# Kernel tuning notes

Hardware: AMD Instinct MI355X
Metric: run time of the kernel (lower is better)

The kernel has to match this reference:

```python
import jax, jax.numpy as jnp
import numpy as np

EMB = 768
HEADS = 12
HD = EMB // HEADS
FF = 4 * EMB
EPS = 1e-5


def gelu_tanh(x):
    c = jnp.sqrt(jnp.asarray(2.0 / jnp.pi, x.dtype))
    return 0.5 * x * (1.0 + jnp.tanh(c * (x + 0.044715 * x ** 3)))


def layernorm(x, scale, shift):
    mean = x.mean(-1, keepdims=True)
    var = ((x - mean) ** 2).mean(-1, keepdims=True)
    return scale * (x - mean) / jnp.sqrt(var + EPS) + shift


def setup_inputs() -> dict:
    key = jax.random.key(0)
    ks = jax.random.split(key, 12)
    s = 0.02
    return {
        "x": jax.random.normal(ks[0], (8, 1024, EMB), jnp.float32),
        "Wq": jax.random.normal(ks[1], (EMB, EMB), jnp.float32) * s,
        "Wk": jax.random.normal(ks[2], (EMB, EMB), jnp.float32) * s,
        "Wv": jax.random.normal(ks[3], (EMB, EMB), jnp.float32) * s,
        "Wo": jax.random.normal(ks[4], (EMB, EMB), jnp.float32) * s,
        "bo": jnp.zeros((EMB,), jnp.float32),
        "W1": jax.random.normal(ks[5], (EMB, FF), jnp.float32) * s,
        "b1": jnp.zeros((FF,), jnp.float32),
        "W2": jax.random.normal(ks[6], (FF, EMB), jnp.float32) * s,
        "b2": jnp.zeros((EMB,), jnp.float32),
        "ln1_scale": jnp.ones((EMB,), jnp.float32),
        "ln1_shift": jnp.zeros((EMB,), jnp.float32),
        "ln2_scale": jnp.ones((EMB,), jnp.float32),
        "ln2_shift": jnp.zeros((EMB,), jnp.float32),
    }


def reference(x, Wq, Wk, Wv, Wo, bo, W1, b1, W2, b2,
              ln1_scale, ln1_shift, ln2_scale, ln2_shift):
    B, T, _ = x.shape
    inp = x
    h = layernorm(x, ln1_scale, ln1_shift)
    # QKV projections (no bias, qkv_bias=False)
    q = (h @ Wq).reshape(B, T, HEADS, HD).transpose(0, 2, 1, 3)  # [B,H,T,hd]
    k = (h @ Wk).reshape(B, T, HEADS, HD).transpose(0, 2, 1, 3)
    v = (h @ Wv).reshape(B, T, HEADS, HD).transpose(0, 2, 1, 3)
    scores = jnp.einsum('bhqd,bhkd->bhqk', q, k)
    causal = jnp.triu(jnp.ones((T, T), bool), k=1)
    scores = jnp.where(causal, -jnp.inf, scores)
    attn = jax.nn.softmax(scores / jnp.sqrt(jnp.asarray(HD, x.dtype)), axis=-1)
    ctx = jnp.einsum('bhqk,bhkd->bhqd', attn, v)
    ctx = ctx.transpose(0, 2, 1, 3).reshape(B, T, EMB)
    attn_out = ctx @ Wo + bo
    x = inp + attn_out  # dropout is identity (rate 0 / eval)
    inp = x
    h = layernorm(x, ln2_scale, ln2_shift)
    ff = gelu_tanh(h @ W1 + b1) @ W2 + b2
    return inp + ff
```

## Files before the change

### kernel.cpp

```cpp
#include <hip/hip_runtime.h>
#include <stdint.h>
#include <stddef.h>

#define EMB 768
#define FFD 3072
#define NHEAD 12
#define HD 64
#define SEQ 1024
#define NTOK 8192
#define QKVW 2304

typedef unsigned short u16;
typedef __attribute__((ext_vector_type(8))) short short8;
typedef __attribute__((ext_vector_type(4))) float f32x4;

__device__ __forceinline__ u16 f2bf(float f) {
  union { float f; uint32_t u; } w; w.f = f;
  uint32_t x = w.u + 0x7fffu + ((w.u >> 16) & 1u);
  return (u16)(x >> 16);
}

__device__ __forceinline__ void g2l16(const void* g, void* l) {
  __builtin_amdgcn_global_load_lds(
      (const __attribute__((address_space(1))) void*)g,
      (__attribute__((address_space(3))) void*)l, 16, 0, 0);
}

__global__ __launch_bounds__(256)
void transpose_kernel(const float* __restrict__ in, u16* __restrict__ out, int K, int N) {
  __shared__ float tile[32][33];
  const int n0 = blockIdx.x * 32, k0 = blockIdx.y * 32;
  const int tx = threadIdx.x & 31;
  const int ty = threadIdx.x >> 5;
#pragma unroll
  for (int i = 0; i < 32; i += 8)
    tile[ty + i][tx] = in[(size_t)(k0 + ty + i) * N + n0 + tx];
  __syncthreads();
#pragma unroll
  for (int i = 0; i < 32; i += 8)
    out[(size_t)(n0 + ty + i) * K + k0 + tx] = f2bf(tile[tx][ty + i]);
}

__global__ __launch_bounds__(256)
void transpose_qkv_kernel(const float* __restrict__ Wq, const float* __restrict__ Wk,
                          const float* __restrict__ Wv, u16* __restrict__ out) {
  __shared__ float tile[32][33];
  const float* in = blockIdx.z == 0 ? Wq : (blockIdx.z == 1 ? Wk : Wv);
  u16* o = out + (size_t)blockIdx.z * EMB * EMB;
  const int n0 = blockIdx.x * 32, k0 = blockIdx.y * 32;
  const int tx = threadIdx.x & 31;
  const int ty = threadIdx.x >> 5;
#pragma unroll
  for (int i = 0; i < 32; i += 8)
    tile[ty + i][tx] = in[(size_t)(k0 + ty + i) * EMB + n0 + tx];
  __syncthreads();
#pragma unroll
  for (int i = 0; i < 32; i += 8)
    o[(size_t)(n0 + ty + i) * EMB + k0 + tx] = f2bf(tile[tx][ty + i]);
}

__global__ __launch_bounds__(256)
void ln_kernel(const float* __restrict__ x, const float* __restrict__ sc,
               const float* __restrict__ sh, u16* __restrict__ out) {
  const int row = blockIdx.x;
  const int tid = threadIdx.x;
  const float* xr = x + (size_t)row * EMB;
  float v0 = xr[tid], v1 = xr[tid + 256], v2 = xr[tid + 512];
  float s = v0 + v1 + v2;
  float ss = v0 * v0 + v1 * v1 + v2 * v2;
#pragma unroll
  for (int m = 1; m < 64; m <<= 1) { s += __shfl_xor(s, m, 64); ss += __shfl_xor(ss, m, 64); }
  __shared__ float red[8];
  const int wave = tid >> 6, lane = tid & 63;
  if (lane == 0) { red[wave] = s; red[wave + 4] = ss; }
  __syncthreads();
  s = red[0] + red[1] + red[2] + red[3];
  ss = red[4] + red[5] + red[6] + red[7];
  const float mean = s * (1.f / EMB);
  const float var = ss * (1.f / EMB) - mean * mean;
  const float inv = rsqrtf(var + 1e-5f);
  u16* orow = out + (size_t)row * EMB;
  orow[tid]       = f2bf((v0 - mean) * inv * sc[tid]       + sh[tid]);
  orow[tid + 256] = f2bf((v1 - mean) * inv * sc[tid + 256] + sh[tid + 256]);
  orow[tid + 512] = f2bf((v2 - mean) * inv * sc[tid + 512] + sh[tid + 512]);
}

template <int EPI, int MT>
__global__ __launch_bounds__(256)
void gemm_kernel(const u16* __restrict__ A, const u16* __restrict__ BT,
                 void* __restrict__ Cp, const float* __restrict__ bias,
                 const float* __restrict__ res, int M, int N, int K) {
  constexpr int MI = MT / 32;
  __shared__ u16 As[MT * 64];
  __shared__ u16 Bs[128 * 64];

  const int nwg = gridDim.x * gridDim.y;
  const int orig = blockIdx.y * gridDim.x + blockIdx.x;
  const int swz = (orig & 7) * (nwg >> 3) + (orig >> 3);
  const int m0 = (swz / gridDim.x) * MT;
  const int n0 = (swz % gridDim.x) * 128;

  const int tid = threadIdx.x;
  const int wave = tid >> 6, lane = tid & 63;
  const int wr = wave >> 1, wc = wave & 1;
  const int r = lane & 15, g = lane >> 4;
  const int lrow = lane >> 3;
  const int lelem = (lane & 7) * 8;

  f32x4 acc[MI][4] = {};

  const int nkt = K >> 6;
  for (int kt = 0; kt < nkt; ++kt) {
    const int k0 = kt << 6;
    if (kt) __syncthreads();
#pragma unroll
    for (int q = 0; q < MT / 32; ++q) {
      const int chunk = q * 4 + wave;
      const int row = chunk * 8 + lrow;
      const int e = lelem ^ ((row & 7) << 3);
      g2l16(A + (size_t)(m0 + row) * K + k0 + e, As + chunk * 512);
    }
#pragma unroll
    for (int q = 0; q < 4; ++q) {
      const int chunk = q * 4 + wave;
      const int row = chunk * 8 + lrow;
      const int e = lelem ^ ((row & 7) << 3);
      g2l16(BT + (size_t)(n0 + row) * K + k0 + e, Bs + chunk * 512);
    }
    __syncthreads();
#pragma unroll
    for (int kk = 0; kk < 2; ++kk) {
      short8 af[MI], bf[4];
#pragma unroll
      for (int mi = 0; mi < MI; ++mi) {
        const int row = wr * (MT / 2) + mi * 16 + r;
        af[mi] = *(const short8*)(As + row * 64 + ((kk * 32 + g * 8) ^ ((row & 7) << 3)));
      }
#pragma unroll
      for (int ni = 0; ni < 4; ++ni) {
        const int row = wc * 64 + ni * 16 + r;
        bf[ni] = *(const short8*)(Bs + row * 64 + ((kk * 32 + g * 8) ^ ((row & 7) << 3)));
      }
#pragma unroll
      for (int mi = 0; mi < MI; ++mi)
#pragma unroll
        for (int ni = 0; ni < 4; ++ni)
          acc[mi][ni] = __builtin_amdgcn_mfma_f32_16x16x32_bf16(af[mi], bf[ni], acc[mi][ni], 0, 0, 0);
    }
  }

#pragma unroll
  for (int mi = 0; mi < MI; ++mi)
#pragma unroll
    for (int ni = 0; ni < 4; ++ni)
#pragma unroll
      for (int j = 0; j < 4; ++j) {
        const int row = m0 + wr * (MT / 2) + mi * 16 + 4 * g + j;
        const int col = n0 + wc * 64 + ni * 16 + r;
        const size_t idx = (size_t)row * N + col;
        float v = acc[mi][ni][j];
        if constexpr (EPI == 0) {
          ((u16*)Cp)[idx] = f2bf(v);
        } else if constexpr (EPI == 1) {
          ((float*)Cp)[idx] = v + bias[col] + res[idx];
        } else {
          float t = v + bias[col];
          float e = __expf(1.5957691216057308f * (t + 0.044715f * t * t * t));
          float th = 1.f - 2.f / (e + 1.f);
          ((u16*)Cp)[idx] = f2bf(0.5f * t * (1.f + th));
        }
      }
}

__global__ __launch_bounds__(256)
void attn_kernel(const u16* __restrict__ qkv, u16* __restrict__ ctx) {
  const int bh = blockIdx.x;
  const int qt = blockIdx.y;
  const int b = bh / NHEAD, h = bh % NHEAD;
  const int tid = threadIdx.x;
  const int wave = tid >> 6, lane = tid & 63;
  const int r = lane & 15, g = lane >> 4;

  __shared__ u16 Kl[64 * 64];
  __shared__ u16 Vt[64 * 64];
  __shared__ u16 Pl[4][16 * 64];

  const int qrow0 = b * SEQ + qt * 64 + wave * 16;
  const u16* qbase = qkv + (size_t)(qrow0 + r) * QKVW + h * HD;
  short8 aq0 = *(const short8*)(qbase + g * 8);
  short8 aq1 = *(const short8*)(qbase + 32 + g * 8);

  float mrow[4], lrow[4];
  f32x4 oc[4] = {};
#pragma unroll
  for (int j = 0; j < 4; ++j) { mrow[j] = -1e30f; lrow[j] = 0.f; }

  const int kvrow0 = b * SEQ;
  for (int kb = 0; kb <= qt; ++kb) {
    if (kb) __syncthreads();
#pragma unroll
    for (int q = 0; q < 2; ++q) {
      const int c = tid + q * 256;
      const int kr = c >> 3;
      const int kc = (c & 7) << 3;
      const u16* gk = qkv + (size_t)(kvrow0 + kb * 64 + kr) * QKVW + EMB + h * HD + kc;
      short8 kv = *(const short8*)gk;
      *(short8*)((char*)Kl + kr * 128 + ((kc * 2) ^ ((kr & 7) << 4))) = kv;
      const u16* gv = gk + EMB;
      short8 vv = *(const short8*)gv;
#pragma unroll
      for (int e = 0; e < 8; ++e) {
        const int d = kc + e;
        *((u16*)((char*)Vt + d * 128 + ((kr * 2) ^ ((d & 7) << 4)))) = (u16)vv[e];
      }
    }
    __syncthreads();

    f32x4 s[4];
#pragma unroll
    for (int nf = 0; nf < 4; ++nf) {
      f32x4 z = {};
      const int krow = nf * 16 + r;
#pragma unroll
      for (int seg = 0; seg < 2; ++seg) {
        short8 bk = *(const short8*)((const char*)Kl + krow * 128 +
                                     ((seg * 64 + g * 16) ^ ((krow & 7) << 4)));
        z = __builtin_amdgcn_mfma_f32_16x16x32_bf16(seg ? aq1 : aq0, bk, z, 0, 0, 0);
      }
      s[nf] = z;
    }

    float pv[4][4];
    const bool diag = (kb == qt);
#pragma unroll
    for (int nf = 0; nf < 4; ++nf)
#pragma unroll
      for (int j = 0; j < 4; ++j) {
        float sv = s[nf][j] * 0.125f;
        if (diag && (nf * 16 + r) > (wave * 16 + 4 * g + j)) sv = -1e30f;
        pv[nf][j] = sv;
      }

#pragma unroll
    for (int j = 0; j < 4; ++j) {
      float mx = fmaxf(fmaxf(pv[0][j], pv[1][j]), fmaxf(pv[2][j], pv[3][j]));
#pragma unroll
      for (int sh = 1; sh < 16; sh <<= 1) mx = fmaxf(mx, __shfl_xor(mx, sh, 64));
      const float mn = fmaxf(mrow[j], mx);
      const float alpha = __expf(mrow[j] - mn);
      float ps = 0.f;
#pragma unroll
      for (int nf = 0; nf < 4; ++nf) {
        const float p = __expf(pv[nf][j] - mn);
        pv[nf][j] = p;
        ps += p;
      }
#pragma unroll
      for (int sh = 1; sh < 16; sh <<= 1) ps += __shfl_xor(ps, sh, 64);
      lrow[j] = lrow[j] * alpha + ps;
      mrow[j] = mn;
#pragma unroll
      for (int nd = 0; nd < 4; ++nd) oc[nd][j] *= alpha;
    }

    u16* Pw = (u16*)Pl[wave];
#pragma unroll
    for (int nf = 0; nf < 4; ++nf)
#pragma unroll
      for (int j = 0; j < 4; ++j) {
        const int pr = 4 * g + j;
        *((u16*)((char*)Pw + pr * 128 + (((nf * 16 + r) * 2) ^ ((pr & 7) << 4)))) = f2bf(pv[nf][j]);
      }
    short8 pa0 = *(const short8*)((const char*)Pw + r * 128 + ((g * 16) ^ ((r & 7) << 4)));
    short8 pa1 = *(const short8*)((const char*)Pw + r * 128 + ((64 + g * 16) ^ ((r & 7) << 4)));

#pragma unroll
    for (int nd = 0; nd < 4; ++nd) {
      const int vr = nd * 16 + r;
#pragma unroll
      for (int seg = 0; seg < 2; ++seg) {
        short8 bv = *(const short8*)((const char*)Vt + vr * 128 +
                                     ((seg * 64 + g * 16) ^ ((vr & 7) << 4)));
        oc[nd] = __builtin_amdgcn_mfma_f32_16x16x32_bf16(seg ? pa1 : pa0, bv, oc[nd], 0, 0, 0);
      }
    }
  }

#pragma unroll
  for (int nd = 0; nd < 4; ++nd)
#pragma unroll
    for (int j = 0; j < 4; ++j) {
      const size_t row = (size_t)qrow0 + 4 * g + j;
      ctx[row * EMB + h * HD + nd * 16 + r] = f2bf(oc[nd][j] / lrow[j]);
    }
}

extern "C" void kernel_launch(void* const* d_in, const int* in_sizes, int n_in,
                              void* d_out, int out_size, void* d_ws, size_t ws_size,
                              hipStream_t stream) {
  const float* x    = (const float*)d_in[0];
  const float* Wq   = (const float*)d_in[1];
  const float* Wk   = (const float*)d_in[2];
  const float* Wv   = (const float*)d_in[3];
  const float* Wo   = (const float*)d_in[4];
  const float* bo   = (const float*)d_in[5];
  const float* W1   = (const float*)d_in[6];
  const float* b1   = (const float*)d_in[7];
  const float* W2   = (const float*)d_in[8];
  const float* b2   = (const float*)d_in[9];
  const float* ln1s = (const float*)d_in[10];
  const float* ln1b = (const float*)d_in[11];
  const float* ln2s = (const float*)d_in[12];
  const float* ln2b = (const float*)d_in[13];

  char* p = (char*)d_ws;
  u16* qkvT = (u16*)p; p += (size_t)QKVW * EMB * 2;
  u16* woT  = (u16*)p; p += (size_t)EMB * EMB * 2;
  u16* w1T  = (u16*)p; p += (size_t)FFD * EMB * 2;
  u16* w2T  = (u16*)p; p += (size_t)EMB * FFD * 2;
  u16* h1   = (u16*)p; p += (size_t)NTOK * EMB * 2;
  u16* qkv  = (u16*)p; p += (size_t)NTOK * QKVW * 2;
  float* x2 = (float*)p; p += (size_t)NTOK * EMB * 4;
  u16* ff1  = (u16*)p; p += (size_t)NTOK * FFD * 2;
  u16* ctxb = h1;
  u16* h2   = qkv;

  if (ws_size < (size_t)(p - (char*)d_ws)) return;

  dim3 blk(256);
  transpose_qkv_kernel<<<dim3(24, 24, 3), blk, 0, stream>>>(Wq, Wk, Wv, qkvT);
  transpose_kernel<<<dim3(24, 24), blk, 0, stream>>>(Wo, woT, EMB, EMB);
  transpose_kernel<<<dim3(96, 24), blk, 0, stream>>>(W1, w1T, EMB, FFD);
  transpose_kernel<<<dim3(24, 96), blk, 0, stream>>>(W2, w2T, FFD, EMB);

  ln_kernel<<<NTOK, blk, 0, stream>>>(x, ln1s, ln1b, h1);
  gemm_kernel<0, 128><<<dim3(18, 64), blk, 0, stream>>>(h1, qkvT, qkv, nullptr, nullptr, NTOK, QKVW, EMB);
  attn_kernel<<<dim3(96, 16), blk, 0, stream>>>(qkv, ctxb);
  gemm_kernel<1, 64><<<dim3(6, 128), blk, 0, stream>>>(ctxb, woT, x2, bo, x, NTOK, EMB, EMB);
  ln_kernel<<<NTOK, blk, 0, stream>>>(x2, ln2s, ln2b, h2);
  gemm_kernel<2, 128><<<dim3(24, 64), blk, 0, stream>>>(h2, w1T, ff1, b1, nullptr, NTOK, FFD, EMB);
  gemm_kernel<1, 64><<<dim3(6, 128), blk, 0, stream>>>(ff1, w2T, (float*)d_out, b2, x2, NTOK, EMB, FFD);
}
```

Measured before the change: 266.8 us.

## Restructure attention with 128-row query tiles, transposed S, register prefetch, lazy rescale

The attention kernel now processes 128 query rows per block (32 per wave, two 16-row fragments), so each K/V tile loaded into LDS serves twice as many queries and the grid drops from 16 to 8 query tiles. It computes S transposed so the softmax reductions need only two cross-lane shuffles. The next K/V tile is prefetched into registers while the current one is computed, and V gets an extra XOR swizzle for the transposed stores. Softmax uses exp2 with a folded scale and skips rescaling unless the row max grows past a threshold, and P is written to LDS as packed bf16 pairs. The cost is more registers per thread and fewer, longer blocks with a worse causal load imbalance.

After: 261.6 us. About the same (-2.0%).

```diff
diff --git a/kernel.cpp b/kernel.cpp
--- a/kernel.cpp
+++ b/kernel.cpp
@@ -1,4 +1,5 @@
 #include <hip/hip_runtime.h>
+#include <hip/hip_bf16.h>
 #include <stdint.h>
 #include <stddef.h>
 
@@ -18,6 +19,12 @@
   union { float f; uint32_t u; } w; w.f = f;
   uint32_t x = w.u + 0x7fffu + ((w.u >> 16) & 1u);
   return (u16)(x >> 16);
+}
+
+__device__ __forceinline__ uint32_t pkbf(float lo, float hi) {
+  __hip_bfloat162 h = __float22bfloat162_rn(float2{lo, hi});
+  union { __hip_bfloat162 h; uint32_t u; } cv; cv.h = h;
+  return cv.u;
 }
 
 __device__ __forceinline__ void g2l16(const void* g, void* l) {
@@ -172,6 +179,9 @@
       }
 }
 
+#define CEXP 0.18033688011112042f
+#define DMTHR 64.0f
+
 __global__ __launch_bounds__(256)
 void attn_kernel(const u16* __restrict__ qkv, u16* __restrict__ ctx) {
   const int bh = blockIdx.x;
@@ -183,116 +193,164 @@
 
   __shared__ u16 Kl[64 * 64];
   __shared__ u16 Vt[64 * 64];
-  __shared__ u16 Pl[4][16 * 64];
-
-  const int qrow0 = b * SEQ + qt * 64 + wave * 16;
-  const u16* qbase = qkv + (size_t)(qrow0 + r) * QKVW + h * HD;
-  short8 aq0 = *(const short8*)(qbase + g * 8);
-  short8 aq1 = *(const short8*)(qbase + 32 + g * 8);
-
-  float mrow[4], lrow[4];
-  f32x4 oc[4] = {};
-#pragma unroll
-  for (int j = 0; j < 4; ++j) { mrow[j] = -1e30f; lrow[j] = 0.f; }
-
-  const int kvrow0 = b * SEQ;
-  for (int kb = 0; kb <= qt; ++kb) {
-    if (kb) __syncthreads();
-#pragma unroll
-    for (int q = 0; q < 2; ++q) {
-      const int c = tid + q * 256;
-      const int kr = c >> 3;
-      const int kc = (c & 7) << 3;
-      const u16* gk = qkv + (size_t)(kvrow0 + kb * 64 + kr) * QKVW + EMB + h * HD + kc;
-      short8 kv = *(const short8*)gk;
-      *(short8*)((char*)Kl + kr * 128 + ((kc * 2) ^ ((kr & 7) << 4))) = kv;
-      const u16* gv = gk + EMB;
-      short8 vv = *(const short8*)gv;
+  __shared__ u16 Pt[4][16 * 64];
+
+  const int q0 = qt * 128;
+  const int qw = q0 + wave * 32;
+  const int tok0 = b * SEQ;
+
+  short8 aq[2][2];
+#pragma unroll
+  for (int qf = 0; qf < 2; ++qf) {
+    const u16* qb = qkv + (size_t)(tok0 + qw + qf * 16 + r) * QKVW + h * HD;
+    aq[qf][0] = *(const short8*)(qb + g * 8);
+    aq[qf][1] = *(const short8*)(qb + 32 + g * 8);
+  }
+
+  float m_st[2] = {-1e30f, -1e30f};
+  float l_st[2] = {0.f, 0.f};
+  f32x4 oc[2][4] = {};
+
+  const int sr = tid >> 3;
+  const int sc = (tid & 7) * 8;
+  const int nt = 2 * qt + 2;
+
+  short8 kreg[2], vreg[2];
+  {
+    const u16* kb0 = qkv + (size_t)(tok0 + sr) * QKVW + EMB + h * HD + sc;
+    kreg[0] = *(const short8*)kb0;
+    vreg[0] = *(const short8*)(kb0 + EMB);
+    kreg[1] = *(const short8*)(kb0 + 32 * QKVW);
+    vreg[1] = *(const short8*)(kb0 + 32 * QKVW + EMB);
+  }
+
+  for (int kb = 0; kb < nt; ++kb) {
+    __syncthreads();
+#pragma unroll
+    for (int it = 0; it < 2; ++it) {
+      const int row = sr + it * 32;
+      *(short8*)((char*)Kl + row * 128 + ((sc * 2) ^ ((row & 7) << 4))) = kreg[it];
 #pragma unroll
       for (int e = 0; e < 8; ++e) {
-        const int d = kc + e;
-        *((u16*)((char*)Vt + d * 128 + ((kr * 2) ^ ((d & 7) << 4)))) = (u16)vv[e];
+        const int d = sc + e;
+        *((u16*)((char*)Vt + d * 128 +
+                 ((row * 2) ^ ((((d & 7) ^ ((d >> 3) & 7))) << 4)))) = (u16)vreg[it][e];
       }
     }
     __syncthreads();
-
-    f32x4 s[4];
+    if (kb + 1 < nt) {
+      const u16* kb0 = qkv + (size_t)(tok0 + (kb + 1) * 64 + sr) * QKVW + EMB + h * HD + sc;
+      kreg[0] = *(const short8*)kb0;
+      vreg[0] = *(const short8*)(kb0 + EMB);
+      kreg[1] = *(const short8*)(kb0 + 32 * QKVW);
+      vreg[1] = *(const short8*)(kb0 + 32 * QKVW + EMB);
+    }
+
+    const int kv0 = kb * 64;
+    if (kv0 > qw + 31) continue;
+
+    short8 kf[4][2];
 #pragma unroll
     for (int nf = 0; nf < 4; ++nf) {
-      f32x4 z = {};
-      const int krow = nf * 16 + r;
-#pragma unroll
-      for (int seg = 0; seg < 2; ++seg) {
-        short8 bk = *(const short8*)((const char*)Kl + krow * 128 +
-                                     ((seg * 64 + g * 16) ^ ((krow & 7) << 4)));
-        z = __builtin_amdgcn_mfma_f32_16x16x32_bf16(seg ? aq1 : aq0, bk, z, 0, 0, 0);
-      }
-      s[nf] = z;
-    }
-
-    float pv[4][4];
-    const bool diag = (kb == qt);
-#pragma unroll
-    for (int nf = 0; nf < 4; ++nf)
-#pragma unroll
-      for (int j = 0; j < 4; ++j) {
-        float sv = s[nf][j] * 0.125f;
-        if (diag && (nf * 16 + r) > (wave * 16 + 4 * g + j)) sv = -1e30f;
-        pv[nf][j] = sv;
-      }
-
+      const int row = nf * 16 + r;
+#pragma unroll
+      for (int kk = 0; kk < 2; ++kk)
+        kf[nf][kk] = *(const short8*)((char*)Kl + row * 128 +
+                                      ((kk * 64 + g * 16) ^ ((row & 7) << 4)));
+    }
+    short8 bv[2][4];
+#pragma unroll
+    for (int half = 0; half < 2; ++half)
+#pragma unroll
+      for (int nd = 0; nd < 4; ++nd) {
+        const int vr = nd * 16 + r;
+        bv[half][nd] = *(const short8*)((char*)Vt + vr * 128 +
+                       ((half * 64 + g * 16) ^ ((((vr & 7) ^ ((vr >> 3) & 7))) << 4)));
+      }
+
+#pragma unroll
+    for (int qf = 0; qf < 2; ++qf) {
+      f32x4 st[4];
+#pragma unroll
+      for (int nf = 0; nf < 4; ++nf) {
+        f32x4 z = {};
+        z = __builtin_amdgcn_mfma_f32_16x16x32_bf16(kf[nf][0], aq[qf][0], z, 0, 0, 0);
+        z = __builtin_amdgcn_mfma_f32_16x16x32_bf16(kf[nf][1], aq[qf][1], z, 0, 0, 0);
+        st[nf] = z;
+      }
+      const int qg = qw + qf * 16 + r;
+      if (kv0 + 63 > qw + qf * 16) {
+#pragma unroll
+        for (int nf = 0; nf < 4; ++nf)
+#pragma unroll
+          for (int j = 0; j < 4; ++j)
+            if (kv0 + nf * 16 + 4 * g + j > qg) st[nf][j] = -3e38f;
+      }
+      float mx = st[0][0];
+#pragma unroll
+      for (int nf = 0; nf < 4; ++nf)
+#pragma unroll
+        for (int j = 0; j < 4; ++j) mx = fmaxf(mx, st[nf][j]);
+      mx = fmaxf(mx, __shfl_xor(mx, 16));
+      mx = fmaxf(mx, __shfl_xor(mx, 32));
+
+      if (!__all(mx - m_st[qf] <= DMTHR)) {
+        const float mn = fmaxf(m_st[qf], mx);
+        const float al = exp2f((m_st[qf] - mn) * CEXP);
+        m_st[qf] = mn;
+        l_st[qf] *= al;
+#pragma unroll
+        for (int j = 0; j < 4; ++j) {
+          const float aj = __shfl(al, 4 * g + j, 16);
+#pragma unroll
+          for (int nd = 0; nd < 4; ++nd) oc[qf][nd][j] *= aj;
+        }
+      }
+      float p[4][4];
+      float ps = 0.f;
+#pragma unroll
+      for (int nf = 0; nf < 4; ++nf)
+#pragma unroll
+        for (int j = 0; j < 4; ++j) {
+          const float pe = exp2f((st[nf][j] - m_st[qf]) * CEXP);
+          p[nf][j] = pe;
+          ps += pe;
+        }
+      ps += __shfl_xor(ps, 16);
+      ps += __shfl_xor(ps, 32);
+      l_st[qf] += ps;
+
+      u16* Pw = (u16*)Pt[wave];
+#pragma unroll
+      for (int nf = 0; nf < 4; ++nf) {
+        uint2 w2;
+        w2.x = pkbf(p[nf][0], p[nf][1]);
+        w2.y = pkbf(p[nf][2], p[nf][3]);
+        *(uint2*)((char*)Pw + r * 128 + ((nf * 32 + g * 8) ^ ((r & 7) << 4))) = w2;
+      }
+#pragma unroll
+      for (int half = 0; half < 2; ++half) {
+        short8 pa = *(const short8*)((char*)Pw + r * 128 +
+                                     ((half * 64 + g * 16) ^ ((r & 7) << 4)));
+#pragma unroll
+        for (int nd = 0; nd < 4; ++nd)
+          oc[qf][nd] = __builtin_amdgcn_mfma_f32_16x16x32_bf16(pa, bv[half][nd], oc[qf][nd], 0, 0, 0);
+      }
+    }
+  }
+
+#pragma unroll
+  for (int qf = 0; qf < 2; ++qf) {
+    const float rl = 1.f / l_st[qf];
 #pragma unroll
     for (int j = 0; j < 4; ++j) {
-      float mx = fmaxf(fmaxf(pv[0][j], pv[1][j]), fmaxf(pv[2][j], pv[3][j]));
-#pragma unroll
-      for (int sh = 1; sh < 16; sh <<= 1) mx = fmaxf(mx, __shfl_xor(mx, sh, 64));
-      const float mn = fmaxf(mrow[j], mx);
-      const float alpha = __expf(mrow[j] - mn);
-      float ps = 0.f;
-#pragma unroll
-      for (int nf = 0; nf < 4; ++nf) {
-        const float p = __expf(pv[nf][j] - mn);
-        pv[nf][j] = p;
-        ps += p;
-      }
-#pragma unroll
-      for (int sh = 1; sh < 16; sh <<= 1) ps += __shfl_xor(ps, sh, 64);
-      lrow[j] = lrow[j] * alpha + ps;
-      mrow[j] = mn;
-#pragma unroll
-      for (int nd = 0; nd < 4; ++nd) oc[nd][j] *= alpha;
-    }
-
-    u16* Pw = (u16*)Pl[wave];
-#pragma unroll
-    for (int nf = 0; nf < 4; ++nf)
-#pragma unroll
-      for (int j = 0; j < 4; ++j) {
-        const int pr = 4 * g + j;
-        *((u16*)((char*)Pw + pr * 128 + (((nf * 16 + r) * 2) ^ ((pr & 7) << 4)))) = f2bf(pv[nf][j]);
-      }
-    short8 pa0 = *(const short8*)((const char*)Pw + r * 128 + ((g * 16) ^ ((r & 7) << 4)));
-    short8 pa1 = *(const short8*)((const char*)Pw + r * 128 + ((64 + g * 16) ^ ((r & 7) << 4)));
-
-#pragma unroll
-    for (int nd = 0; nd < 4; ++nd) {
-      const int vr = nd * 16 + r;
-#pragma unroll
-      for (int seg = 0; seg < 2; ++seg) {
-        short8 bv = *(const short8*)((const char*)Vt + vr * 128 +
-                                     ((seg * 64 + g * 16) ^ ((vr & 7) << 4)));
-        oc[nd] = __builtin_amdgcn_mfma_f32_16x16x32_bf16(seg ? pa1 : pa0, bv, oc[nd], 0, 0, 0);
-      }
+      const float rj = __shfl(rl, 4 * g + j, 16);
+      const size_t row = (size_t)tok0 + qw + qf * 16 + 4 * g + j;
+#pragma unroll
+      for (int nd = 0; nd < 4; ++nd)
+        ctx[row * EMB + h * HD + nd * 16 + r] = f2bf(oc[qf][nd][j] * rj);
     }
   }
-
-#pragma unroll
-  for (int nd = 0; nd < 4; ++nd)
-#pragma unroll
-    for (int j = 0; j < 4; ++j) {
-      const size_t row = (size_t)qrow0 + 4 * g + j;
-      ctx[row * EMB + h * HD + nd * 16 + r] = f2bf(oc[nd][j] / lrow[j]);
-    }
 }
 
 extern "C" void kernel_launch(void* const* d_in, const int* in_sizes, int n_in,
@@ -335,7 +393,7 @@
 
   ln_kernel<<<NTOK, blk, 0, stream>>>(x, ln1s, ln1b, h1);
   gemm_kernel<0, 128><<<dim3(18, 64), blk, 0, stream>>>(h1, qkvT, qkv, nullptr, nullptr, NTOK, QKVW, EMB);
-  attn_kernel<<<dim3(96, 16), blk, 0, stream>>>(qkv, ctxb);
+  attn_kernel<<<dim3(96, 8), blk, 0, stream>>>(qkv, ctxb);
   gemm_kernel<1, 64><<<dim3(6, 128), blk, 0, stream>>>(ctxb, woT, x2, bo, x, NTOK, EMB, EMB);
   ln_kernel<<<NTOK, blk, 0, stream>>>(x2, ln2s, ln2b, h2);
   gemm_kernel<2, 128><<<dim3(24, 64), blk, 0, stream>>>(h2, w1T, ff1, b1, nullptr, NTOK, FFD, EMB);
```
